# Optimization experiments

Hardware: AMD Instinct MI355X
Metric: run time of the kernel (lower is better)

The kernel has to match this reference:

```python
import jax, jax.numpy as jnp
import numpy as np

NUM_EMBEDDINGS = 1024
EMBEDDING_DIM = 256
COMMITMENT_COST = 0.25


def setup_inputs() -> dict:
    key = jax.random.key(0)
    kx, ke = jax.random.split(key)
    x = jax.random.normal(kx, (8, EMBEDDING_DIM, 16, 32, 32), dtype=jnp.float32)
    emb = jax.random.uniform(ke, (NUM_EMBEDDINGS, EMBEDDING_DIM), dtype=jnp.float32,
                             minval=-1.0 / NUM_EMBEDDINGS, maxval=1.0 / NUM_EMBEDDINGS)
    return {"x": x, "emb": emb}


def reference(x, emb):
    sg = jax.lax.stop_gradient
    # x: [B, C, T, H, W] -> channels-last [B, T, H, W, C]
    x_flat = jnp.transpose(x, (0, 2, 3, 4, 1))
    flat = x_flat.reshape(-1, EMBEDDING_DIM)  # [N, D]
    # squared L2 distances to each codeword: [N, K]
    distances = (jnp.sum(flat ** 2, axis=1, keepdims=True)
                 + jnp.sum(emb ** 2, axis=1)
                 - 2.0 * flat @ emb.T)
    encoding_indices = jnp.argmin(distances, axis=1)  # [N]
    # one-hot @ codebook == direct gather
    quantized = emb[encoding_indices].reshape(x_flat.shape)
    loss = (jnp.mean((sg(quantized) - x_flat) ** 2)
            + COMMITMENT_COST * jnp.mean((quantized - sg(x_flat)) ** 2))
    # straight-through estimator
    quantized_st = x_flat + sg(quantized - x_flat)
    return jnp.transpose(quantized_st, (0, 4, 1, 2, 3)), loss
```

## Files before the change

### kernel.cpp

```cpp
#include <hip/hip_runtime.h>
#include <hip/hip_bf16.h>
#include <stdint.h>

#define N_TOT    131072
#define DIM      256
#define KCODES   1024
#define THW      16384
#define OUT_ELEMS 33554432ULL

typedef short short8 __attribute__((ext_vector_type(8)));
typedef float f32x4  __attribute__((ext_vector_type(4)));

__device__ __forceinline__ unsigned short f2bf_rne(float f) {
  union { float f; unsigned int u; } c; c.f = f;
  unsigned int u = c.u;
  unsigned int r = u + 0x7FFFu + ((u >> 16) & 1u);
  return (unsigned short)(r >> 16);
}

__device__ __forceinline__ void async_cp16(void* lds, const void* gsrc) {
  __builtin_amdgcn_global_load_lds(
      (const __attribute__((address_space(1))) void*)gsrc,
      (__attribute__((address_space(3))) void*)lds, 16, 0, 0);
}

__global__ __launch_bounds__(64) void k_prep(const float* __restrict__ emb,
                                             unsigned short* __restrict__ embB,
                                             float* __restrict__ e2,
                                             float* __restrict__ lossAcc) {
  const int k = blockIdx.x;
  const int t = threadIdx.x;
  const float4 v = ((const float4*)(emb + (size_t)k * DIM))[t];
  float s = v.x * v.x + v.y * v.y + v.z * v.z + v.w * v.w;
  ushort4 bv;
  bv.x = f2bf_rne(v.x); bv.y = f2bf_rne(v.y);
  bv.z = f2bf_rne(v.z); bv.w = f2bf_rne(v.w);
  const int c0 = 4 * t;
  const int ks = c0 >> 5, q = (c0 >> 3) & 3, j0 = c0 & 7;
  const int lane = q * 16 + (k & 15);
  unsigned short* dst = embB + (size_t)((((k >> 4) * 8 + ks) * 64 + lane) * 8 + j0);
  *(ushort4*)dst = bv;
  #pragma unroll
  for (int m = 32; m; m >>= 1) s += __shfl_xor(s, m, 64);
  if (t == 0) e2[k] = s;
  if (k == 0 && t == 0) *lossAcc = 0.0f;
}

__global__ __launch_bounds__(256) void k_gemm_argmin(
    const float* __restrict__ x, const unsigned short* __restrict__ embB,
    const float* __restrict__ e2, int* __restrict__ idxOut,
    float* __restrict__ lossAcc) {
  __shared__ __align__(16) unsigned short eT[2][16384];

  const int tid  = threadIdx.x;
  const int wave = tid >> 6;
  const int lane = tid & 63;
  const int q    = lane >> 4;
  const int l15  = lane & 15;
  const int nw0  = blockIdx.x * 128 + wave * 32;
  const int b    = nw0 >> 14;

  {
    const char* gsrc = (const char*)embB;
    char* ldst = (char*)&eT[0][0];
    #pragma unroll
    for (int kk = 0; kk < 8; ++kk)
      async_cp16(ldst + (tid + kk * 256) * 16, gsrc + (size_t)(tid + kk * 256) * 16);
  }

  short8 A[2][8];
  float x2sum = 0.0f;
  #pragma unroll
  for (int mf = 0; mf < 2; ++mf) {
    const int n   = nw0 + mf * 16 + l15;
    const int thw = n & (THW - 1);
    const float* __restrict__ xr = x + (size_t)b * DIM * THW + thw;
    #pragma unroll
    for (int ks = 0; ks < 8; ++ks) {
      const int c0 = ks * 32 + q * 8;
      short8 a;
      #pragma unroll
      for (int j = 0; j < 8; ++j) {
        float v = xr[(size_t)(c0 + j) * THW];
        x2sum += v * v;
        a[j] = (short)f2bf_rne(-2.0f * v);
      }
      A[mf][ks] = a;
    }
  }

  float mins[2][4];
  int   mini[2][4];
  #pragma unroll
  for (int mf = 0; mf < 2; ++mf)
    #pragma unroll
    for (int r = 0; r < 4; ++r) { mins[mf][r] = 3.4e38f; mini[mf][r] = 0; }

  __syncthreads();

  for (int ch = 0; ch < 16; ++ch) {
    if (ch + 1 < 16) {
      const char* gsrc = (const char*)embB + (size_t)(ch + 1) * 32768;
      char* ldst = (char*)&eT[(ch + 1) & 1][0];
      #pragma unroll
      for (int kk = 0; kk < 8; ++kk)
        async_cp16(ldst + (tid + kk * 256) * 16, gsrc + (size_t)(tid + kk * 256) * 16);
    }
    const unsigned short* __restrict__ buf = &eT[ch & 1][0];
    const int cb = ch * 64;

    #pragma unroll
    for (int cgl = 0; cgl < 4; ++cgl) {
      short8 B[8];
      #pragma unroll
      for (int ks = 0; ks < 8; ++ks)
        B[ks] = *(const short8*)(buf + (size_t)(((cgl * 8 + ks) * 64 + lane) * 8));
      const int   cod = cb + cgl * 16 + l15;
      const float e2v = e2[cod];

      f32x4 acc0 = {0.f, 0.f, 0.f, 0.f};
      f32x4 acc1 = {0.f, 0.f, 0.f, 0.f};
      #pragma unroll
      for (int ks = 0; ks < 8; ++ks) {
        acc0 = __builtin_amdgcn_mfma_f32_16x16x32_bf16(A[0][ks], B[ks], acc0, 0, 0, 0);
        acc1 = __builtin_amdgcn_mfma_f32_16x16x32_bf16(A[1][ks], B[ks], acc1, 0, 0, 0);
      }
      #pragma unroll
      for (int r = 0; r < 4; ++r) {
        float s0 = acc0[r] + e2v;
        if (s0 < mins[0][r]) { mins[0][r] = s0; mini[0][r] = cod; }
        float s1 = acc1[r] + e2v;
        if (s1 < mins[1][r]) { mins[1][r] = s1; mini[1][r] = cod; }
      }
    }
    __syncthreads();
  }

  #pragma unroll
  for (int m = 1; m <= 8; m <<= 1) {
    #pragma unroll
    for (int mf = 0; mf < 2; ++mf)
      #pragma unroll
      for (int r = 0; r < 4; ++r) {
        float os = __shfl_xor(mins[mf][r], m, 64);
        int   oi = __shfl_xor(mini[mf][r], m, 64);
        if (os < mins[mf][r] || (os == mins[mf][r] && oi < mini[mf][r])) {
          mins[mf][r] = os; mini[mf][r] = oi;
        }
      }
  }

  float sstar = 0.0f;
  if (l15 == 0) {
    #pragma unroll
    for (int mf = 0; mf < 2; ++mf)
      #pragma unroll
      for (int r = 0; r < 4; ++r) {
        idxOut[nw0 + mf * 16 + q * 4 + r] = mini[mf][r];
        sstar += mins[mf][r];
      }
  }
  float tot = x2sum + sstar;
  #pragma unroll
  for (int m = 32; m; m >>= 1) tot += __shfl_xor(tot, m, 64);
  if (lane == 0) atomicAdd(lossAcc, tot);
}

#define TSTR 65
__global__ __launch_bounds__(256) void k_out(
    const float* __restrict__ emb, const int* __restrict__ idx,
    float* __restrict__ out, const float* __restrict__ lossAcc) {
  __shared__ __align__(16) float tile[256 * TSTR];
  const int tid  = threadIdx.x;
  const int wave = tid >> 6;
  const int lane = tid & 63;
  const int l15  = lane & 15;
  const int n0   = blockIdx.x * 256;

  if (blockIdx.x == 0 && tid == 0)
    out[OUT_ELEMS] = 1.25f * lossAcc[0] * (1.0f / (float)OUT_ELEMS);

  const int myid = idx[n0 + tid];
  const int b    = n0 >> 14;
  const int thw0 = n0 & (THW - 1);
  float* __restrict__ ob = out + (size_t)b * DIM * THW + thw0;
  const float* __restrict__ er = emb + (size_t)myid * DIM;

  for (int cc = 0; cc < 4; ++cc) {
    const int c0 = cc * 64;
    #pragma unroll
    for (int j = 0; j < 16; ++j) {
      const float4 v = *(const float4*)(er + c0 + 4 * j);
      *(float4*)&tile[tid * TSTR + 4 * j] = v;
    }
    __syncthreads();
    #pragma unroll
    for (int ci = 0; ci < 16; ++ci) {
      const int dc = (lane >> 4) + 4 * ci;
      const int nl = wave * 64 + 4 * l15;
      float4 v;
      v.x = tile[(nl + 0) * TSTR + dc];
      v.y = tile[(nl + 1) * TSTR + dc];
      v.z = tile[(nl + 2) * TSTR + dc];
      v.w = tile[(nl + 3) * TSTR + dc];
      *(float4*)(ob + (size_t)(c0 + dc) * THW + nl) = v;
    }
    __syncthreads();
  }
}

extern "C" void kernel_launch(void* const* d_in, const int* in_sizes, int n_in,
                              void* d_out, int out_size, void* d_ws, size_t ws_size,
                              hipStream_t stream) {
  const float* x   = (const float*)d_in[0];
  const float* emb = (const float*)d_in[1];
  float* out = (float*)d_out;
  char* ws = (char*)d_ws;

  unsigned short* embB = (unsigned short*)(ws);
  float* e2      = (float*)(ws + 524288);
  int*   idx     = (int*)(ws + 528384);
  float* lossAcc = (float*)(ws + 1052672);

  k_prep<<<KCODES, 64, 0, stream>>>(emb, embB, e2, lossAcc);
  k_gemm_argmin<<<N_TOT / 128, 256, 0, stream>>>(x, embB, e2, idx, lossAcc);
  k_out<<<N_TOT / 256, 256, 0, stream>>>(emb, idx, out, lossAcc);
}
```

Baseline: 361.7 us.

## Pack argmin index into float bits, enlarge GEMM blocks, simplify output scatter

The argmin kernel now uses 512-thread blocks covering 256 rows, so each codebook chunk staged in LDS serves twice as many rows. It keeps a single packed float per slot, with the code index in the low 10 mantissa bits, so a plain fminf does the compare-and-select and the cross-lane reduction. Per-chunk e2 loads are hoisted. The output kernel drops the LDS transpose and writes directly with coalesced per-channel stores. Truncating mantissa bits slightly perturbs distances and tie-breaking, which can change chosen indices and the loss.

```diff
diff --git a/kernel.cpp b/kernel.cpp
--- a/kernel.cpp
+++ b/kernel.cpp
@@ -46,7 +46,7 @@
   if (k == 0 && t == 0) *lossAcc = 0.0f;
 }
 
-__global__ __launch_bounds__(256) void k_gemm_argmin(
+__global__ __launch_bounds__(512, 4) void k_gemm_argmin(
     const float* __restrict__ x, const unsigned short* __restrict__ embB,
     const float* __restrict__ e2, int* __restrict__ idxOut,
     float* __restrict__ lossAcc) {
@@ -57,15 +57,15 @@
   const int lane = tid & 63;
   const int q    = lane >> 4;
   const int l15  = lane & 15;
-  const int nw0  = blockIdx.x * 128 + wave * 32;
+  const int nw0  = blockIdx.x * 256 + wave * 32;
   const int b    = nw0 >> 14;
 
   {
     const char* gsrc = (const char*)embB;
     char* ldst = (char*)&eT[0][0];
     #pragma unroll
-    for (int kk = 0; kk < 8; ++kk)
-      async_cp16(ldst + (tid + kk * 256) * 16, gsrc + (size_t)(tid + kk * 256) * 16);
+    for (int kk = 0; kk < 4; ++kk)
+      async_cp16(ldst + (tid + kk * 512) * 16, gsrc + (size_t)(tid + kk * 512) * 16);
   }
 
   short8 A[2][8];
@@ -89,12 +89,11 @@
     }
   }
 
-  float mins[2][4];
-  int   mini[2][4];
+  float pmin[2][4];
   #pragma unroll
   for (int mf = 0; mf < 2; ++mf)
     #pragma unroll
-    for (int r = 0; r < 4; ++r) { mins[mf][r] = 3.4e38f; mini[mf][r] = 0; }
+    for (int r = 0; r < 4; ++r) pmin[mf][r] = 3.4e38f;
 
   __syncthreads();
 
@@ -103,20 +102,22 @@
       const char* gsrc = (const char*)embB + (size_t)(ch + 1) * 32768;
       char* ldst = (char*)&eT[(ch + 1) & 1][0];
       #pragma unroll
-      for (int kk = 0; kk < 8; ++kk)
-        async_cp16(ldst + (tid + kk * 256) * 16, gsrc + (size_t)(tid + kk * 256) * 16);
+      for (int kk = 0; kk < 4; ++kk)
+        async_cp16(ldst + (tid + kk * 512) * 16, gsrc + (size_t)(tid + kk * 512) * 16);
     }
     const unsigned short* __restrict__ buf = &eT[ch & 1][0];
     const int cb = ch * 64;
 
+    float e2c[4];
+    #pragma unroll
+    for (int g = 0; g < 4; ++g) e2c[g] = e2[cb + g * 16 + l15];
+
     #pragma unroll
     for (int cgl = 0; cgl < 4; ++cgl) {
       short8 B[8];
       #pragma unroll
       for (int ks = 0; ks < 8; ++ks)
         B[ks] = *(const short8*)(buf + (size_t)(((cgl * 8 + ks) * 64 + lane) * 8));
-      const int   cod = cb + cgl * 16 + l15;
-      const float e2v = e2[cod];
 
       f32x4 acc0 = {0.f, 0.f, 0.f, 0.f};
       f32x4 acc1 = {0.f, 0.f, 0.f, 0.f};
@@ -125,30 +126,28 @@
         acc0 = __builtin_amdgcn_mfma_f32_16x16x32_bf16(A[0][ks], B[ks], acc0, 0, 0, 0);
         acc1 = __builtin_amdgcn_mfma_f32_16x16x32_bf16(A[1][ks], B[ks], acc1, 0, 0, 0);
       }
+      const unsigned int cod = (unsigned int)(cb + cgl * 16 + l15);
+      const float e2v = e2c[cgl];
       #pragma unroll
       for (int r = 0; r < 4; ++r) {
-        float s0 = acc0[r] + e2v;
-        if (s0 < mins[0][r]) { mins[0][r] = s0; mini[0][r] = cod; }
-        float s1 = acc1[r] + e2v;
-        if (s1 < mins[1][r]) { mins[1][r] = s1; mini[1][r] = cod; }
+        float d0 = acc0[r] + e2v;
+        unsigned int u0 = (__float_as_uint(d0) & 0xFFFFFC00u) | cod;
+        pmin[0][r] = fminf(pmin[0][r], __uint_as_float(u0));
+        float d1 = acc1[r] + e2v;
+        unsigned int u1 = (__float_as_uint(d1) & 0xFFFFFC00u) | cod;
+        pmin[1][r] = fminf(pmin[1][r], __uint_as_float(u1));
       }
     }
     __syncthreads();
   }
 
   #pragma unroll
-  for (int m = 1; m <= 8; m <<= 1) {
+  for (int m = 1; m <= 8; m <<= 1)
     #pragma unroll
     for (int mf = 0; mf < 2; ++mf)
       #pragma unroll
-      for (int r = 0; r < 4; ++r) {
-        float os = __shfl_xor(mins[mf][r], m, 64);
-        int   oi = __shfl_xor(mini[mf][r], m, 64);
-        if (os < mins[mf][r] || (os == mins[mf][r] && oi < mini[mf][r])) {
-          mins[mf][r] = os; mini[mf][r] = oi;
-        }
-      }
-  }
+      for (int r = 0; r < 4; ++r)
+        pmin[mf][r] = fminf(pmin[mf][r], __shfl_xor(pmin[mf][r], m, 64));
 
   float sstar = 0.0f;
   if (l15 == 0) {
@@ -156,8 +155,9 @@
     for (int mf = 0; mf < 2; ++mf)
       #pragma unroll
       for (int r = 0; r < 4; ++r) {
-        idxOut[nw0 + mf * 16 + q * 4 + r] = mini[mf][r];
-        sstar += mins[mf][r];
+        const unsigned int u = __float_as_uint(pmin[mf][r]);
+        idxOut[nw0 + mf * 16 + q * 4 + r] = (int)(u & 1023u);
+        sstar += __uint_as_float(u & 0xFFFFFC00u);
       }
   }
   float tot = x2sum + sstar;
@@ -166,46 +166,28 @@
   if (lane == 0) atomicAdd(lossAcc, tot);
 }
 
-#define TSTR 65
 __global__ __launch_bounds__(256) void k_out(
     const float* __restrict__ emb, const int* __restrict__ idx,
     float* __restrict__ out, const float* __restrict__ lossAcc) {
-  __shared__ __align__(16) float tile[256 * TSTR];
-  const int tid  = threadIdx.x;
-  const int wave = tid >> 6;
-  const int lane = tid & 63;
-  const int l15  = lane & 15;
-  const int n0   = blockIdx.x * 256;
+  const int tid = threadIdx.x;
+  const int n   = blockIdx.x * 256 + tid;
 
   if (blockIdx.x == 0 && tid == 0)
     out[OUT_ELEMS] = 1.25f * lossAcc[0] * (1.0f / (float)OUT_ELEMS);
 
-  const int myid = idx[n0 + tid];
-  const int b    = n0 >> 14;
-  const int thw0 = n0 & (THW - 1);
-  float* __restrict__ ob = out + (size_t)b * DIM * THW + thw0;
-  const float* __restrict__ er = emb + (size_t)myid * DIM;
-
-  for (int cc = 0; cc < 4; ++cc) {
-    const int c0 = cc * 64;
-    #pragma unroll
-    for (int j = 0; j < 16; ++j) {
-      const float4 v = *(const float4*)(er + c0 + 4 * j);
-      *(float4*)&tile[tid * TSTR + 4 * j] = v;
-    }
-    __syncthreads();
-    #pragma unroll
-    for (int ci = 0; ci < 16; ++ci) {
-      const int dc = (lane >> 4) + 4 * ci;
-      const int nl = wave * 64 + 4 * l15;
-      float4 v;
-      v.x = tile[(nl + 0) * TSTR + dc];
-      v.y = tile[(nl + 1) * TSTR + dc];
-      v.z = tile[(nl + 2) * TSTR + dc];
-      v.w = tile[(nl + 3) * TSTR + dc];
-      *(float4*)(ob + (size_t)(c0 + dc) * THW + nl) = v;
-    }
-    __syncthreads();
+  const int id  = idx[n];
+  const int b   = n >> 14;
+  const int thw = n & (THW - 1);
+  const float* __restrict__ er = emb + (size_t)id * DIM;
+  float* __restrict__ ob = out + (size_t)b * DIM * THW + thw;
+
+  #pragma unroll 8
+  for (int cq = 0; cq < 64; ++cq) {
+    const float4 v = ((const float4*)er)[cq];
+    ob[(size_t)(4 * cq + 0) * THW] = v.x;
+    ob[(size_t)(4 * cq + 1) * THW] = v.y;
+    ob[(size_t)(4 * cq + 2) * THW] = v.z;
+    ob[(size_t)(4 * cq + 3) * THW] = v.w;
   }
 }
 
@@ -223,6 +205,6 @@
   float* lossAcc = (float*)(ws + 1052672);
 
   k_prep<<<KCODES, 64, 0, stream>>>(emb, embB, e2, lossAcc);
-  k_gemm_argmin<<<N_TOT / 128, 256, 0, stream>>>(x, embB, e2, idx, lossAcc);
+  k_gemm_argmin<<<N_TOT / 256, 512, 0, stream>>>(x, embB, e2, idx, lossAcc);
   k_out<<<N_TOT / 256, 256, 0, stream>>>(emb, idx, out, lossAcc);
 }
```

Measured after the change: 424.3 us. 1.17x slower.

## Widen argmin tile to 64 rows per wave and pack index into distance bits

Applied to the files above, without the earlier changes.

Each wave now handles four 16-row MFMA fragments instead of two, so every LDS codebook fragment feeds twice as many MFMAs and the grid is halved. The running argmin becomes one packed float per row: the low 10 mantissa bits of the distance are replaced by the code index, so a single fminf replaces the compare-and-select on separate value and index registers, including in the cross-lane reduction. Codeword norms for a chunk are loaded once up front, and launch bounds ask for 2 blocks per CU. The wider tile raises register pressure, and the packing truncates distances, which can change tie-breaking, gives wrong ordering when distances are negative, and lowers loss precision slightly.

```diff
diff --git a/kernel.cpp b/kernel.cpp
--- a/kernel.cpp
+++ b/kernel.cpp
@@ -46,7 +46,7 @@
   if (k == 0 && t == 0) *lossAcc = 0.0f;
 }
 
-__global__ __launch_bounds__(256) void k_gemm_argmin(
+__global__ __launch_bounds__(256, 2) void k_gemm_argmin(
     const float* __restrict__ x, const unsigned short* __restrict__ embB,
     const float* __restrict__ e2, int* __restrict__ idxOut,
     float* __restrict__ lossAcc) {
@@ -57,7 +57,7 @@
   const int lane = tid & 63;
   const int q    = lane >> 4;
   const int l15  = lane & 15;
-  const int nw0  = blockIdx.x * 128 + wave * 32;
+  const int nw0  = blockIdx.x * 256 + wave * 64;
   const int b    = nw0 >> 14;
 
   {
@@ -68,10 +68,10 @@
       async_cp16(ldst + (tid + kk * 256) * 16, gsrc + (size_t)(tid + kk * 256) * 16);
   }
 
-  short8 A[2][8];
+  short8 A[4][8];
   float x2sum = 0.0f;
   #pragma unroll
-  for (int mf = 0; mf < 2; ++mf) {
+  for (int mf = 0; mf < 4; ++mf) {
     const int n   = nw0 + mf * 16 + l15;
     const int thw = n & (THW - 1);
     const float* __restrict__ xr = x + (size_t)b * DIM * THW + thw;
@@ -89,12 +89,11 @@
     }
   }
 
-  float mins[2][4];
-  int   mini[2][4];
-  #pragma unroll
-  for (int mf = 0; mf < 2; ++mf)
-    #pragma unroll
-    for (int r = 0; r < 4; ++r) { mins[mf][r] = 3.4e38f; mini[mf][r] = 0; }
+  float pmin[4][4];
+  #pragma unroll
+  for (int mf = 0; mf < 4; ++mf)
+    #pragma unroll
+    for (int r = 0; r < 4; ++r) pmin[mf][r] = 3.4e38f;
 
   __syncthreads();
 
@@ -109,55 +108,58 @@
     const unsigned short* __restrict__ buf = &eT[ch & 1][0];
     const int cb = ch * 64;
 
+    float e2c[4];
+    #pragma unroll
+    for (int g = 0; g < 4; ++g) e2c[g] = e2[cb + g * 16 + l15];
+
     #pragma unroll
     for (int cgl = 0; cgl < 4; ++cgl) {
       short8 B[8];
       #pragma unroll
       for (int ks = 0; ks < 8; ++ks)
         B[ks] = *(const short8*)(buf + (size_t)(((cgl * 8 + ks) * 64 + lane) * 8));
-      const int   cod = cb + cgl * 16 + l15;
-      const float e2v = e2[cod];
-
-      f32x4 acc0 = {0.f, 0.f, 0.f, 0.f};
-      f32x4 acc1 = {0.f, 0.f, 0.f, 0.f};
+
+      f32x4 acc[4];
+      #pragma unroll
+      for (int mf = 0; mf < 4; ++mf) acc[mf] = (f32x4){0.f, 0.f, 0.f, 0.f};
       #pragma unroll
       for (int ks = 0; ks < 8; ++ks) {
-        acc0 = __builtin_amdgcn_mfma_f32_16x16x32_bf16(A[0][ks], B[ks], acc0, 0, 0, 0);
-        acc1 = __builtin_amdgcn_mfma_f32_16x16x32_bf16(A[1][ks], B[ks], acc1, 0, 0, 0);
-      }
-      #pragma unroll
-      for (int r = 0; r < 4; ++r) {
-        float s0 = acc0[r] + e2v;
-        if (s0 < mins[0][r]) { mins[0][r] = s0; mini[0][r] = cod; }
-        float s1 = acc1[r] + e2v;
-        if (s1 < mins[1][r]) { mins[1][r] = s1; mini[1][r] = cod; }
+        #pragma unroll
+        for (int mf = 0; mf < 4; ++mf)
+          acc[mf] = __builtin_amdgcn_mfma_f32_16x16x32_bf16(A[mf][ks], B[ks], acc[mf], 0, 0, 0);
+      }
+      const unsigned int cod = (unsigned int)(cb + cgl * 16 + l15);
+      const float e2v = e2c[cgl];
+      #pragma unroll
+      for (int mf = 0; mf < 4; ++mf) {
+        #pragma unroll
+        for (int r = 0; r < 4; ++r) {
+          float d = acc[mf][r] + e2v;
+          unsigned int u = (__float_as_uint(d) & 0xFFFFFC00u) | cod;
+          pmin[mf][r] = fminf(pmin[mf][r], __uint_as_float(u));
+        }
       }
     }
     __syncthreads();
   }
 
   #pragma unroll
-  for (int m = 1; m <= 8; m <<= 1) {
-    #pragma unroll
-    for (int mf = 0; mf < 2; ++mf)
-      #pragma unroll
-      for (int r = 0; r < 4; ++r) {
-        float os = __shfl_xor(mins[mf][r], m, 64);
-        int   oi = __shfl_xor(mini[mf][r], m, 64);
-        if (os < mins[mf][r] || (os == mins[mf][r] && oi < mini[mf][r])) {
-          mins[mf][r] = os; mini[mf][r] = oi;
-        }
-      }
-  }
+  for (int m = 1; m <= 8; m <<= 1)
+    #pragma unroll
+    for (int mf = 0; mf < 4; ++mf)
+      #pragma unroll
+      for (int r = 0; r < 4; ++r)
+        pmin[mf][r] = fminf(pmin[mf][r], __shfl_xor(pmin[mf][r], m, 64));
 
   float sstar = 0.0f;
   if (l15 == 0) {
     #pragma unroll
-    for (int mf = 0; mf < 2; ++mf)
+    for (int mf = 0; mf < 4; ++mf)
       #pragma unroll
       for (int r = 0; r < 4; ++r) {
-        idxOut[nw0 + mf * 16 + q * 4 + r] = mini[mf][r];
-        sstar += mins[mf][r];
+        const unsigned int u = __float_as_uint(pmin[mf][r]);
+        idxOut[nw0 + mf * 16 + q * 4 + r] = (int)(u & 1023u);
+        sstar += __uint_as_float(u & 0xFFFFFC00u);
       }
   }
   float tot = x2sum + sstar;
@@ -223,6 +225,6 @@
   float* lossAcc = (float*)(ws + 1052672);
 
   k_prep<<<KCODES, 64, 0, stream>>>(emb, embB, e2, lossAcc);
-  k_gemm_argmin<<<N_TOT / 128, 256, 0, stream>>>(x, embB, e2, idx, lossAcc);
+  k_gemm_argmin<<<N_TOT / 256, 256, 0, stream>>>(x, embB, e2, idx, lossAcc);
   k_out<<<N_TOT / 256, 256, 0, stream>>>(emb, idx, out, lossAcc);
 }
```

Result: slower. 425.6 us (+17.7%).
